# Kernel tuning notes

Hardware: AMD Instinct MI355X
Metric: run time of the kernel (lower is better)

## Reference

```python
import jax, jax.numpy as jnp
import numpy as np

E = 8            # n_experts
TEMP = float(np.e)
N_ACTIVE = 5     # max(1, int(8 * 0.7))
EPS = 1e-8


def setup_inputs() -> dict:
    key = jax.random.key(0)
    ks = jax.random.split(key, 6)
    N, D, H, O = 8192, 1024, 2048, 1024

    def init(k, shape, fan_in):
        return (jax.random.normal(k, shape, jnp.float32) / np.sqrt(fan_in)).astype(jnp.float32)

    return {
        "x": jax.random.normal(ks[0], (N, D), jnp.float32),
        "gate_W": init(ks[1], (D, E), D),
        "gate_b": jnp.zeros((E,), jnp.float32),
        "W1": init(ks[2], (E, D, H), D),
        "b1": jnp.zeros((E, H), jnp.float32),
        "W2": init(ks[3], (E, H, H), H),
        "b2": jnp.zeros((E, H), jnp.float32),
        "W3": init(ks[4], (E, H, O), H),
        "b3": jnp.zeros((E, O), jnp.float32),
    }


def reference(x, gate_W, gate_b, W1, b1, W2, b2, W3, b3):
    # Boltzmann gate: softmax(scores / T), keep top n_active, renormalize.
    scores = (x @ gate_W + gate_b) / TEMP            # [N, E]
    probs = jax.nn.softmax(scores, axis=-1)          # [N, E]
    _, idx = jax.lax.top_k(probs, N_ACTIVE)          # [N, n_active]
    rows = jnp.arange(probs.shape[0])[:, None]
    mask = jnp.zeros_like(probs).at[rows, idx].set(1.0)
    w = probs * mask
    w = w / (w.sum(axis=-1, keepdims=True) + EPS)    # [N, E]

    # Dense all-expert MLP (dropout is identity in eval mode).
    h = jax.nn.relu(jnp.einsum('nd,edh->enh', x, W1) + b1[:, None, :])   # [E, N, H]
    h = jax.nn.relu(jnp.einsum('enh,ehk->enk', h, W2) + b2[:, None, :])  # [E, N, H]
    out = jnp.einsum('enh,eho->eno', h, W3) + b3[:, None, :]             # [E, N, O]

    # Weighted combine over experts.
    return jnp.einsum('ne,eno->no', w, out)          # [N, O]
```

## Files before the change

### kernel.cpp

```cpp
#include <hip/hip_runtime.h>

#define N_ROWS 8192
#define DIM_D  1024
#define DIM_H  2048
#define DIM_O  1024
#define NEXP   8
#define NACT   5
#define MT128  336

typedef _Float16 f16x8 __attribute__((ext_vector_type(8)));
typedef float    f32x4 __attribute__((ext_vector_type(4)));

__device__ __forceinline__ void gload_lds16(const void* g, void* l) {
  __builtin_amdgcn_global_load_lds(
      (const __attribute__((address_space(1))) void*)g,
      (__attribute__((address_space(3))) void*)l, 16, 0, 0);
}

__global__ void convert_x_kernel(const float* __restrict__ in,
                                 _Float16* __restrict__ out, int n) {
  int i = (blockIdx.x * 256 + threadIdx.x) * 8;
  if (i >= n) return;
  const float4 a = *(const float4*)(in + i);
  const float4 b = *(const float4*)(in + i + 4);
  f16x8 v;
  v[0] = (_Float16)a.x; v[1] = (_Float16)a.y; v[2] = (_Float16)a.z; v[3] = (_Float16)a.w;
  v[4] = (_Float16)b.x; v[5] = (_Float16)b.y; v[6] = (_Float16)b.z; v[7] = (_Float16)b.w;
  *(f16x8*)(out + i) = v;
}

__global__ void zero_f32_kernel(float* __restrict__ p, int n4) {
  int i = blockIdx.x * 256 + threadIdx.x;
  if (i < n4) ((float4*)p)[i] = make_float4(0.f, 0.f, 0.f, 0.f);
}
__global__ void zero_counts_kernel(int* __restrict__ cnt) {
  if (threadIdx.x < NEXP) cnt[threadIdx.x] = 0;
}

__global__ void transpose_to_f16(const float* __restrict__ in,
                                 _Float16* __restrict__ out, int R, int C) {
  in  += (size_t)blockIdx.z * R * C;
  out += (size_t)blockIdx.z * R * C;
  __shared__ float tile[32][33];
  const int tx = threadIdx.x & 31, ty = threadIdx.x >> 5;
  const int c0 = blockIdx.x * 32, r0 = blockIdx.y * 32;
#pragma unroll
  for (int j = 0; j < 32; j += 8)
    tile[ty + j][tx] = in[(size_t)(r0 + ty + j) * C + c0 + tx];
  __syncthreads();
#pragma unroll
  for (int j = 0; j < 32; j += 8)
    out[(size_t)(c0 + ty + j) * R + r0 + tx] = (_Float16)tile[tx][ty + j];
}

__global__ void gate_kernel(const float* __restrict__ x, const float* __restrict__ gW,
                            const float* __restrict__ gb, float* __restrict__ wout) {
  const int lane = threadIdx.x & 63;
  const int row  = blockIdx.x * 4 + (threadIdx.x >> 6);
  float acc[8] = {0.f,0.f,0.f,0.f,0.f,0.f,0.f,0.f};
  const float* xr = x + (size_t)row * DIM_D;
  for (int d = lane; d < DIM_D; d += 64) {
    float xv = xr[d];
    const float4* g4 = (const float4*)(gW + d * 8);
    float4 a = g4[0], b = g4[1];
    acc[0] += xv * a.x; acc[1] += xv * a.y; acc[2] += xv * a.z; acc[3] += xv * a.w;
    acc[4] += xv * b.x; acc[5] += xv * b.y; acc[6] += xv * b.z; acc[7] += xv * b.w;
  }
#pragma unroll
  for (int off = 32; off > 0; off >>= 1) {
#pragma unroll
    for (int e = 0; e < 8; ++e) acc[e] += __shfl_xor(acc[e], off);
  }
  const float invT = 0.36787944117144233f;
  float s[8], mx = -1e30f;
#pragma unroll
  for (int e = 0; e < 8; ++e) { s[e] = (acc[e] + gb[e]) * invT; mx = fmaxf(mx, s[e]); }
  float p[8], sum = 0.f;
#pragma unroll
  for (int e = 0; e < 8; ++e) { p[e] = expf(s[e] - mx); sum += p[e]; }
  float inv = 1.f / sum;
#pragma unroll
  for (int e = 0; e < 8; ++e) p[e] *= inv;
  unsigned keep = 0;
  for (int it = 0; it < NACT; ++it) {
    int best = 0; float bv = -1.f;
#pragma unroll
    for (int e = 0; e < 8; ++e)
      if (!(keep & (1u << e)) && p[e] > bv) { bv = p[e]; best = e; }
    keep |= 1u << best;
  }
  float ks = 0.f;
#pragma unroll
  for (int e = 0; e < 8; ++e) if (keep & (1u << e)) ks += p[e];
  const float winv = 1.f / (ks + 1e-8f);
  if (lane < 8)
    wout[(size_t)row * 8 + lane] = (keep & (1u << lane)) ? p[lane] * winv : 0.f;
}

__global__ void count_kernel(const float* __restrict__ wg, int* __restrict__ cnt) {
  const int row = blockIdx.x * 256 + threadIdx.x;
  const int lane = threadIdx.x & 63;
#pragma unroll
  for (int e = 0; e < NEXP; ++e) {
    const bool keep = wg[(size_t)row * 8 + e] > 0.f;
    unsigned long long m = __ballot(keep);
    if (lane == 0 && m) atomicAdd(&cnt[e], __popcll(m));
  }
}

__global__ void offsets_kernel(const int* __restrict__ cnt, int* __restrict__ cursor,
                               int* __restrict__ offs, int* __restrict__ ntiles,
                               int2* __restrict__ ttab, int* __restrict__ rlist) {
  __shared__ int soffs[NEXP], scnt[NEXP];
  if (threadIdx.x == 0) {
    int off = 0, k = 0;
    for (int e = 0; e < NEXP; ++e) {
      offs[e] = off; soffs[e] = off; scnt[e] = cnt[e];
      cursor[e] = 0;
      const int nt = (cnt[e] + 127) >> 7;
      for (int t2 = 0; t2 < nt; ++t2) { ttab[k] = make_int2(e, off + t2 * 128); ++k; }
      off += nt << 7;
    }
    *ntiles = k;
  }
  __syncthreads();
#pragma unroll
  for (int e = 0; e < NEXP; ++e) {
    const int lo = soffs[e] + scnt[e];
    const int hi = soffs[e] + ((scnt[e] + 127) & ~127);
    for (int i = lo + (int)threadIdx.x; i < hi; i += 256) rlist[i] = 0;
  }
}

__global__ void place_kernel(const float* __restrict__ wg, const int* __restrict__ offs,
                             int* __restrict__ cursor, int* __restrict__ rlist,
                             int* __restrict__ pos) {
  const int row = blockIdx.x * 256 + threadIdx.x;
  const int lane = threadIdx.x & 63;
#pragma unroll
  for (int e = 0; e < NEXP; ++e) {
    const bool keep = wg[(size_t)row * 8 + e] > 0.f;
    unsigned long long m = __ballot(keep);
    if (m) {
      const int leader = __ffsll(m) - 1;
      const int pre = __popcll(m & ((1ull << lane) - 1ull));
      int base = 0;
      if (lane == leader) base = atomicAdd(&cursor[e], __popcll(m));
      base = __shfl(base, leader);
      if (keep) {
        const int idx = offs[e] + base + pre;
        rlist[idx] = row;
        pos[(size_t)row * 8 + e] = idx;
      }
    }
  }
}

__global__ void combine_kernel(const float* __restrict__ wg, const int* __restrict__ pos,
                               const _Float16* __restrict__ y, float* __restrict__ out) {
  const int tid = blockIdx.x * 256 + threadIdx.x;
  const int row = tid >> 7, c8 = (tid & 127) * 8;
  float a[8] = {0.f,0.f,0.f,0.f,0.f,0.f,0.f,0.f};
#pragma unroll
  for (int e = 0; e < NEXP; ++e) {
    const float w = wg[(size_t)row * 8 + e];
    if (w > 0.f) {
      const int p = pos[(size_t)row * 8 + e];
      const f16x8 v = *(const f16x8*)(y + (size_t)p * DIM_O + c8);
#pragma unroll
      for (int j = 0; j < 8; ++j) a[j] += w * (float)v[j];
    }
  }
  float4* o4 = (float4*)(out + (size_t)row * DIM_O + c8);
  o4[0] = make_float4(a[0], a[1], a[2], a[3]);
  o4[1] = make_float4(a[4], a[5], a[6], a[7]);
}

#define MFMA16 __builtin_amdgcn_mfma_f32_16x16x32_f16
template <int MODE>
__global__ __launch_bounds__(256, 4) void gemm128(
    const _Float16* __restrict__ A, const _Float16* __restrict__ BtAll,
    _Float16* __restrict__ C, const float* __restrict__ biasAll,
    const int* __restrict__ rlist, const int2* __restrict__ ttab,
    const int* __restrict__ ntilesp, int N, int K) {
  const int ncol = gridDim.x;
  const int b = blockIdx.y * ncol + blockIdx.x;
  const int xcd = b & 7, idx = b >> 3;
  const int ti = xcd * (MT128 / 8) + idx / ncol;
  const int colt = idx % ncol;
  if (ti >= *ntilesp) return;
  const int2 tt = ttab[ti];
  const int e = tt.x, grow0 = tt.y;
  const int col0 = colt * 128;

  __shared__ _Float16 sA[128 * 64];
  __shared__ _Float16 sB[128 * 64];
  const int t = threadIdx.x;
  const int w = t >> 6, lane = t & 63;
  const int wm = w >> 1, wn = w & 1;
  const int l15 = lane & 15, lg = lane >> 4;

  const _Float16* Bt = BtAll + (size_t)e * N * K;

  const int cb = (((t & 7) ^ ((t >> 3) & 7))) * 8;
  size_t arow[4], brow[4];
#pragma unroll
  for (int i = 0; i < 4; ++i) {
    const int chunk = i * 256 + t;
    const int r = chunk >> 3;
    const int gr = (MODE == 0) ? rlist[grow0 + r] : (grow0 + r);
    arow[i] = (size_t)gr * K;
    brow[i] = (size_t)(col0 + r) * K;
  }

  const int ck0 = ((lg * 16) ^ ((l15 & 7) << 4)) >> 1;
  const int ck1 = ((64 + lg * 16) ^ ((l15 & 7) << 4)) >> 1;

  f32x4 acc[4][4] = {};

  for (int kt = 0; kt < K; kt += 64) {
    __syncthreads();
#pragma unroll
    for (int i = 0; i < 4; ++i)
      gload_lds16(A + arow[i] + kt + cb, sA + (i * 256 + w * 64) * 8);
#pragma unroll
    for (int i = 0; i < 4; ++i)
      gload_lds16(Bt + brow[i] + kt + cb, sB + (i * 256 + w * 64) * 8);
    __syncthreads();
#pragma unroll
    for (int k2 = 0; k2 < 2; ++k2) {
      const int ck = k2 ? ck1 : ck0;
      f16x8 af[4], bf[4];
#pragma unroll
      for (int m = 0; m < 4; ++m)
        af[m] = *(const f16x8*)(sA + (wm * 64 + m * 16 + l15) * 64 + ck);
#pragma unroll
      for (int n = 0; n < 4; ++n)
        bf[n] = *(const f16x8*)(sB + (wn * 64 + n * 16 + l15) * 64 + ck);
#pragma unroll
      for (int m = 0; m < 4; ++m)
#pragma unroll
        for (int n = 0; n < 4; ++n)
          acc[m][n] = MFMA16(af[m], bf[n], acc[m][n], 0, 0, 0);
    }
  }

  const float* bias = biasAll + (size_t)e * N;
#pragma unroll
  for (int m = 0; m < 4; ++m) {
#pragma unroll
    for (int n = 0; n < 4; ++n) {
      const int gc = col0 + wn * 64 + n * 16 + l15;
      const float bv = bias[gc];
#pragma unroll
      for (int r = 0; r < 4; ++r) {
        const int grow = grow0 + wm * 64 + m * 16 + lg * 4 + r;
        const float v = acc[m][n][r] + bv;
        C[(size_t)grow * N + gc] = (_Float16)((MODE == 2) ? v : fmaxf(v, 0.f));
      }
    }
  }
}

__global__ void compact_old(const float* __restrict__ wg, int* __restrict__ cnt,
                            int* __restrict__ rowlist) {
  const int row = blockIdx.x * 256 + threadIdx.x;
  const int lane = threadIdx.x & 63;
#pragma unroll
  for (int e = 0; e < NEXP; ++e) {
    const float w = wg[(size_t)row * 8 + e];
    const bool keep = (w > 0.f);
    unsigned long long m = __ballot(keep);
    if (m) {
      const int leader = __ffsll(m) - 1;
      const int pre = __popcll(m & ((1ull << lane) - 1ull));
      int base = 0;
      if (lane == leader) base = atomicAdd(&cnt[e], __popcll(m));
      base = __shfl(base, leader);
      if (keep) rowlist[e * N_ROWS + base + pre] = row;
    }
  }
}

template <int MODE>
__global__ __launch_bounds__(256, 2) void gemm_nt(
    const _Float16* __restrict__ A, const _Float16* __restrict__ Bt,
    void* __restrict__ Cout, const float* __restrict__ bias,
    const float* __restrict__ wg, const int* __restrict__ rlist,
    const int* __restrict__ cntp, int e, int N, int K) {
  const int M = *cntp;
  const int row0 = blockIdx.y * 128, col0 = blockIdx.x * 128;
  if (row0 >= M) return;
  __shared__ _Float16 sA[128 * 64];
  __shared__ _Float16 sB[128 * 64];
  const int t = threadIdx.x;
  const int w = t >> 6, lane = t & 63;
  const int wm = w >> 1, wn = w & 1;
  const int l15 = lane & 15, lg = lane >> 4;
  size_t arow[4];
#pragma unroll
  for (int i = 0; i < 4; ++i) {
    const int chunk = i * 256 + t;
    int li = row0 + (chunk >> 3);
    if (li >= M && MODE == 0) li = M - 1;
    const int gr = (MODE == 0) ? rlist[li] : li;
    arow[i] = (size_t)gr * K;
  }
  f32x4 acc[4][4] = {};
  for (int kt = 0; kt < K; kt += 64) {
    __syncthreads();
#pragma unroll
    for (int i = 0; i < 4; ++i) {
      const int chunk = i * 256 + t;
      const int cb = (chunk & 7) * 8;
      gload_lds16(A + arow[i] + kt + cb, sA + (i * 256 + w * 64) * 8);
    }
#pragma unroll
    for (int i = 0; i < 4; ++i) {
      const int chunk = i * 256 + t;
      const int r = chunk >> 3, cb = (chunk & 7) * 8;
      gload_lds16(Bt + (size_t)(col0 + r) * K + kt + cb, sB + (i * 256 + w * 64) * 8);
    }
    __syncthreads();
#pragma unroll
    for (int k2 = 0; k2 < 2; ++k2) {
      f16x8 af[4], bf[4];
#pragma unroll
      for (int m = 0; m < 4; ++m)
        af[m] = *(const f16x8*)(sA + (wm * 64 + m * 16 + l15) * 64 + k2 * 32 + lg * 8);
#pragma unroll
      for (int n = 0; n < 4; ++n)
        bf[n] = *(const f16x8*)(sB + (wn * 64 + n * 16 + l15) * 64 + k2 * 32 + lg * 8);
#pragma unroll
      for (int m = 0; m < 4; ++m)
#pragma unroll
        for (int n = 0; n < 4; ++n)
          acc[m][n] = MFMA16(af[m], bf[n], acc[m][n], 0, 0, 0);
    }
  }
#pragma unroll
  for (int m = 0; m < 4; ++m) {
#pragma unroll
    for (int n = 0; n < 4; ++n) {
      const int gc = col0 + wn * 64 + n * 16 + l15;
      const float bvv = bias[gc];
#pragma unroll
      for (int r = 0; r < 4; ++r) {
        const int gr = row0 + wm * 64 + m * 16 + lg * 4 + r;
        float v = acc[m][n][r] + bvv;
        if (MODE == 3) {
          if (gr < M) {
            const int orow = rlist[gr];
            atomicAdd((float*)Cout + (size_t)orow * N + gc,
                      wg[(size_t)orow * 8 + e] * v);
          }
        } else {
          ((_Float16*)Cout)[(size_t)gr * N + gc] = (_Float16)fmaxf(v, 0.f);
        }
      }
    }
  }
}

extern "C" void kernel_launch(void* const* d_in, const int* in_sizes, int n_in,
                              void* d_out, int out_size, void* d_ws, size_t ws_size,
                              hipStream_t stream) {
  const float* x  = (const float*)d_in[0];
  const float* gW = (const float*)d_in[1];
  const float* gb = (const float*)d_in[2];
  const float* W1 = (const float*)d_in[3];
  const float* b1 = (const float*)d_in[4];
  const float* W2 = (const float*)d_in[5];
  const float* b2 = (const float*)d_in[6];
  const float* W3 = (const float*)d_in[7];
  const float* b3 = (const float*)d_in[8];
  float* out = (float*)d_out;

  char* ws = (char*)d_ws;
  const bool big = (ws_size >= 0x1E100000ULL);

  if (big) {
    float* wgate   = (float*)ws;
    int*   meta    = (int*)(ws + 0x40000);
    int*   cnt     = meta;
    int*   cursor  = meta + 8;
    int*   offs    = meta + 16;
    int*   ntiles  = meta + 24;
    int2*  ttab    = (int2*)(meta + 32);
    int*   pos     = (int*)(ws + 0x80000);
    int*   rlistg  = (int*)(ws + 0xC0000);
    _Float16* xh   = (_Float16*)(ws + 0x100000);
    _Float16* h1   = (_Float16*)(ws + 0x1100000);
    _Float16* h2   = (_Float16*)(ws + 0xB900000);
    _Float16* wt1  = (_Float16*)(ws + 0x16100000);
    _Float16* wt2  = (_Float16*)(ws + 0x18100000);
    _Float16* wt3  = (_Float16*)(ws + 0x1C100000);
    _Float16* y    = h1;

    convert_x_kernel<<<(N_ROWS * DIM_D) / (256 * 8), 256, 0, stream>>>(x, xh, N_ROWS * DIM_D);
    gate_kernel<<<N_ROWS / 4, 256, 0, stream>>>(x, gW, gb, wgate);
    zero_counts_kernel<<<1, 64, 0, stream>>>(cnt);
    count_kernel<<<N_ROWS / 256, 256, 0, stream>>>(wgate, cnt);
    offsets_kernel<<<1, 256, 0, stream>>>(cnt, cursor, offs, ntiles, ttab, rlistg);
    place_kernel<<<N_ROWS / 256, 256, 0, stream>>>(wgate, offs, cursor, rlistg, pos);

    transpose_to_f16<<<dim3(DIM_H / 32, DIM_D / 32, NEXP), 256, 0, stream>>>(W1, wt1, DIM_D, DIM_H);
    transpose_to_f16<<<dim3(DIM_H / 32, DIM_H / 32, NEXP), 256, 0, stream>>>(W2, wt2, DIM_H, DIM_H);
    transpose_to_f16<<<dim3(DIM_O / 32, DIM_H / 32, NEXP), 256, 0, stream>>>(W3, wt3, DIM_H, DIM_O);

    gemm128<0><<<dim3(DIM_H / 128, MT128), 256, 0, stream>>>(
        xh, wt1, h1, b1, rlistg, ttab, ntiles, DIM_H, DIM_D);
    gemm128<1><<<dim3(DIM_H / 128, MT128), 256, 0, stream>>>(
        h1, wt2, h2, b2, rlistg, ttab, ntiles, DIM_H, DIM_H);
    gemm128<2><<<dim3(DIM_O / 128, MT128), 256, 0, stream>>>(
        h2, wt3, y, b3, rlistg, ttab, ntiles, DIM_O, DIM_H);

    combine_kernel<<<(N_ROWS * 128) / 256, 256, 0, stream>>>(wgate, pos, y, out);
  } else {
    float*    wgate = (float*)ws;
    int*      cnt   = (int*)(ws + 0x40000);
    int*      rlist = (int*)(ws + 0x80000);
    _Float16* xh    = (_Float16*)(ws + 0x100000);
    _Float16* h1    = (_Float16*)(ws + 0x1100000);
    _Float16* h2    = (_Float16*)(ws + 0x3100000);
    _Float16* wt1   = (_Float16*)(ws + 0x5100000);
    _Float16* wt2   = (_Float16*)(ws + 0x5500000);
    _Float16* wt3   = (_Float16*)(ws + 0x5D00000);

    convert_x_kernel<<<(N_ROWS * DIM_D) / (256 * 8), 256, 0, stream>>>(x, xh, N_ROWS * DIM_D);
    gate_kernel<<<N_ROWS / 4, 256, 0, stream>>>(x, gW, gb, wgate);
    zero_counts_kernel<<<1, 64, 0, stream>>>(cnt);
    compact_old<<<N_ROWS / 256, 256, 0, stream>>>(wgate, cnt, rlist);
    zero_f32_kernel<<<(N_ROWS * DIM_O / 4 + 255) / 256, 256, 0, stream>>>(out, N_ROWS * DIM_O / 4);

    for (int e = 0; e < NEXP; ++e) {
      transpose_to_f16<<<dim3(DIM_H / 32, DIM_D / 32), 256, 0, stream>>>(
          W1 + (size_t)e * DIM_D * DIM_H, wt1, DIM_D, DIM_H);
      transpose_to_f16<<<dim3(DIM_H / 32, DIM_H / 32), 256, 0, stream>>>(
          W2 + (size_t)e * DIM_H * DIM_H, wt2, DIM_H, DIM_H);
      transpose_to_f16<<<dim3(DIM_O / 32, DIM_H / 32), 256, 0, stream>>>(
          W3 + (size_t)e * DIM_H * DIM_O, wt3, DIM_H, DIM_O);
      const int* ce = cnt + e;
      const int* re = rlist + e * N_ROWS;
      gemm_nt<0><<<dim3(DIM_H / 128, N_ROWS / 128), 256, 0, stream>>>(
          xh, wt1, h1, b1 + (size_t)e * DIM_H, wgate, re, ce, e, DIM_H, DIM_D);
      gemm_nt<1><<<dim3(DIM_H / 128, N_ROWS / 128), 256, 0, stream>>>(
          h1, wt2, h2, b2 + (size_t)e * DIM_H, wgate, re, ce, e, DIM_H, DIM_H);
      gemm_nt<3><<<dim3(DIM_O / 128, N_ROWS / 128), 256, 0, stream>>>(
          h2, wt3, out, b3 + (size_t)e * DIM_O, wgate, re, ce, e, DIM_O, DIM_H);
    }
  }
}
```

Baseline: 888.6 us.

## Enlarge grouped expert GEMM row tile to 256 with 4x1 wave layout

The grouped expert GEMMs now use 256-row by 128-column tiles instead of 128x128. Each wave computes 64x128 with a 4x8 MFMA accumulator grid, which raises arithmetic intensity per LDS load, and the routing tables are padded to 256-row tiles. Occupancy is lowered to 2 blocks per CU, LDS per block grows, row offsets use 32-bit math, and bias loads are hoisted. Padding waste per expert also grows, and register pressure rises with 128 accumulator floats per thread.

```diff
diff --git a/kernel.cpp b/kernel.cpp
--- a/kernel.cpp
+++ b/kernel.cpp
@@ -6,7 +6,7 @@
 #define DIM_O  1024
 #define NEXP   8
 #define NACT   5
-#define MT128  336
+#define MT256  176
 
 typedef _Float16 f16x8 __attribute__((ext_vector_type(8)));
 typedef float    f32x4 __attribute__((ext_vector_type(4)));
@@ -117,9 +117,9 @@
     for (int e = 0; e < NEXP; ++e) {
       offs[e] = off; soffs[e] = off; scnt[e] = cnt[e];
       cursor[e] = 0;
-      const int nt = (cnt[e] + 127) >> 7;
-      for (int t2 = 0; t2 < nt; ++t2) { ttab[k] = make_int2(e, off + t2 * 128); ++k; }
-      off += nt << 7;
+      const int nt = (cnt[e] + 255) >> 8;
+      for (int t2 = 0; t2 < nt; ++t2) { ttab[k] = make_int2(e, off + t2 * 256); ++k; }
+      off += nt << 8;
     }
     *ntiles = k;
   }
@@ -127,7 +127,7 @@
 #pragma unroll
   for (int e = 0; e < NEXP; ++e) {
     const int lo = soffs[e] + scnt[e];
-    const int hi = soffs[e] + ((scnt[e] + 127) & ~127);
+    const int hi = soffs[e] + ((scnt[e] + 255) & ~255);
     for (int i = lo + (int)threadIdx.x; i < hi; i += 256) rlist[i] = 0;
   }
 }
@@ -178,7 +178,7 @@
 
 #define MFMA16 __builtin_amdgcn_mfma_f32_16x16x32_f16
 template <int MODE>
-__global__ __launch_bounds__(256, 4) void gemm128(
+__global__ __launch_bounds__(256, 2) void gemm256(
     const _Float16* __restrict__ A, const _Float16* __restrict__ BtAll,
     _Float16* __restrict__ C, const float* __restrict__ biasAll,
     const int* __restrict__ rlist, const int2* __restrict__ ttab,
@@ -186,76 +186,80 @@
   const int ncol = gridDim.x;
   const int b = blockIdx.y * ncol + blockIdx.x;
   const int xcd = b & 7, idx = b >> 3;
-  const int ti = xcd * (MT128 / 8) + idx / ncol;
+  const int ti = xcd * (MT256 / 8) + idx / ncol;
   const int colt = idx % ncol;
   if (ti >= *ntilesp) return;
   const int2 tt = ttab[ti];
   const int e = tt.x, grow0 = tt.y;
   const int col0 = colt * 128;
 
-  __shared__ _Float16 sA[128 * 64];
+  __shared__ _Float16 sA[256 * 64];
   __shared__ _Float16 sB[128 * 64];
   const int t = threadIdx.x;
-  const int w = t >> 6, lane = t & 63;
-  const int wm = w >> 1, wn = w & 1;
+  const int wm = t >> 6, lane = t & 63;
   const int l15 = lane & 15, lg = lane >> 4;
 
   const _Float16* Bt = BtAll + (size_t)e * N * K;
 
-  const int cb = (((t & 7) ^ ((t >> 3) & 7))) * 8;
-  size_t arow[4], brow[4];
+  const int cb = ((t & 7) ^ ((t >> 3) & 7)) * 8;
+  unsigned arow[8], brow[4];
+#pragma unroll
+  for (int i = 0; i < 8; ++i) {
+    const int r = i * 32 + (t >> 3);
+    const int gr = (MODE == 0) ? rlist[grow0 + r] : (grow0 + r);
+    arow[i] = (unsigned)gr * (unsigned)K;
+  }
 #pragma unroll
   for (int i = 0; i < 4; ++i) {
-    const int chunk = i * 256 + t;
-    const int r = chunk >> 3;
-    const int gr = (MODE == 0) ? rlist[grow0 + r] : (grow0 + r);
-    arow[i] = (size_t)gr * K;
-    brow[i] = (size_t)(col0 + r) * K;
+    const int r = i * 32 + (t >> 3);
+    brow[i] = (unsigned)(col0 + r) * (unsigned)K;
   }
 
   const int ck0 = ((lg * 16) ^ ((l15 & 7) << 4)) >> 1;
   const int ck1 = ((64 + lg * 16) ^ ((l15 & 7) << 4)) >> 1;
 
-  f32x4 acc[4][4] = {};
+  f32x4 acc[4][8] = {};
 
   for (int kt = 0; kt < K; kt += 64) {
     __syncthreads();
 #pragma unroll
+    for (int i = 0; i < 8; ++i)
+      gload_lds16(A + (size_t)arow[i] + kt + cb, sA + (i * 256 + wm * 64) * 8);
+#pragma unroll
     for (int i = 0; i < 4; ++i)
-      gload_lds16(A + arow[i] + kt + cb, sA + (i * 256 + w * 64) * 8);
-#pragma unroll
-    for (int i = 0; i < 4; ++i)
-      gload_lds16(Bt + brow[i] + kt + cb, sB + (i * 256 + w * 64) * 8);
+      gload_lds16(Bt + (size_t)brow[i] + kt + cb, sB + (i * 256 + wm * 64) * 8);
     __syncthreads();
 #pragma unroll
     for (int k2 = 0; k2 < 2; ++k2) {
       const int ck = k2 ? ck1 : ck0;
-      f16x8 af[4], bf[4];
+      f16x8 af[4], bf[8];
 #pragma unroll
       for (int m = 0; m < 4; ++m)
         af[m] = *(const f16x8*)(sA + (wm * 64 + m * 16 + l15) * 64 + ck);
 #pragma unroll
-      for (int n = 0; n < 4; ++n)
-        bf[n] = *(const f16x8*)(sB + (wn * 64 + n * 16 + l15) * 64 + ck);
+      for (int n = 0; n < 8; ++n)
+        bf[n] = *(const f16x8*)(sB + (n * 16 + l15) * 64 + ck);
 #pragma unroll
       for (int m = 0; m < 4; ++m)
 #pragma unroll
-        for (int n = 0; n < 4; ++n)
+        for (int n = 0; n < 8; ++n)
           acc[m][n] = MFMA16(af[m], bf[n], acc[m][n], 0, 0, 0);
     }
   }
 
   const float* bias = biasAll + (size_t)e * N;
+  float bv[8];
+#pragma unroll
+  for (int n = 0; n < 8; ++n) bv[n] = bias[col0 + n * 16 + l15];
 #pragma unroll
   for (int m = 0; m < 4; ++m) {
 #pragma unroll
-    for (int n = 0; n < 4; ++n) {
-      const int gc = col0 + wn * 64 + n * 16 + l15;
-      const float bv = bias[gc];
+    for (int n = 0; n < 8; ++n) {
+      const int gc = col0 + n * 16 + l15;
 #pragma unroll
       for (int r = 0; r < 4; ++r) {
         const int grow = grow0 + wm * 64 + m * 16 + lg * 4 + r;
-        const float v = acc[m][n][r] + bv;
+        const float v = acc[m][n][r] + bv[n];
         C[(size_t)grow * N + gc] = (_Float16)((MODE == 2) ? v : fmaxf(v, 0.f));
       }
     }
@@ -408,11 +412,11 @@
     transpose_to_f16<<<dim3(DIM_H / 32, DIM_H / 32, NEXP), 256, 0, stream>>>(W2, wt2, DIM_H, DIM_H);
     transpose_to_f16<<<dim3(DIM_O / 32, DIM_H / 32, NEXP), 256, 0, stream>>>(W3, wt3, DIM_H, DIM_O);
 
-    gemm128<0><<<dim3(DIM_H / 128, MT128), 256, 0, stream>>>(
+    gemm256<0><<<dim3(DIM_H / 128, MT256), 256, 0, stream>>>(
         xh, wt1, h1, b1, rlistg, ttab, ntiles, DIM_H, DIM_D);
-    gemm128<1><<<dim3(DIM_H / 128, MT128), 256, 0, stream>>>(
+    gemm256<1><<<dim3(DIM_H / 128, MT256), 256, 0, stream>>>(
         h1, wt2, h2, b2, rlistg, ttab, ntiles, DIM_H, DIM_H);
-    gemm128<2><<<dim3(DIM_O / 128, MT128), 256, 0, stream>>>(
+    gemm256<2><<<dim3(DIM_O / 128, MT256), 256, 0, stream>>>(
         h2, wt3, y, b3, rlistg, ttab, ntiles, DIM_O, DIM_H);
 
     combine_kernel<<<(N_ROWS * 128) / 256, 256, 0, stream>>>(wgate, pos, y, out);
```

Result: slower. 968.5 us (+9.0%).
